# Optimization experiments

Measured on AMD Instinct MI355X. Metric: run time of the kernel, lower is better.

The kernel has to match this reference:

```python
import jax, jax.numpy as jnp
import numpy as np

B, S, HID = 1, 2048, 2048
NH, NKV, HD = 32, 8, 64
INTER = 8192
EPS = 1e-6


def rmsnorm(x, w, eps=EPS):
    xf = x.astype(jnp.float32)
    inv = jax.lax.rsqrt(jnp.mean(xf * xf, axis=-1, keepdims=True) + eps)
    return (xf * inv * w).astype(x.dtype)


def rope(x, sin_t, cos_t):
    # x: [B, S, H, D]; sin/cos: [S, D//2]
    sin = sin_t[None, :, None, :]
    cos = cos_t[None, :, None, :]
    d2 = x.shape[-1] // 2
    x0, x1 = x[..., :d2], x[..., d2:]
    return jnp.concatenate((x0 * cos - x1 * sin, x0 * sin + x1 * cos), axis=-1)


def setup_inputs() -> dict:
    key = jax.random.key(0)
    ks = jax.random.split(key, 12)
    hidden_states = jax.random.normal(ks[0], (B, S, HID), dtype=jnp.float32)
    # realistic RoPE tables
    inv_freq = 1.0 / (10000.0 ** (np.arange(0, HD // 2, dtype=np.float32) * 2.0 / HD))
    ang = np.arange(S, dtype=np.float32)[:, None] * inv_freq[None, :]
    sin_table = jnp.asarray(np.sin(ang))
    cos_table = jnp.asarray(np.cos(ang))
    s = 0.02
    return {
        "hidden_states": hidden_states,
        "sin_table": sin_table,
        "cos_table": cos_table,
        "ln1_w": jnp.ones((HID,), jnp.float32),
        "ln2_w": jnp.ones((HID,), jnp.float32),
        "wq": jax.random.normal(ks[1], (HID, NH * HD), jnp.float32) * s,
        "wk": jax.random.normal(ks[2], (HID, NKV * HD), jnp.float32) * s,
        "wv": jax.random.normal(ks[3], (HID, NKV * HD), jnp.float32) * s,
        "wo": jax.random.normal(ks[4], (NH * HD, HID), jnp.float32) * s,
        "w_gate": jax.random.normal(ks[5], (HID, INTER), jnp.float32) * s,
        "w_up": jax.random.normal(ks[6], (HID, INTER), jnp.float32) * s,
        "w_down": jax.random.normal(ks[7], (INTER, HID), jnp.float32) * s,
    }


def attention(x, sin_t, cos_t, wq, wk, wv, wo):
    b, s, _ = x.shape
    q = (x @ wq).reshape(b, s, NH, HD)
    k = (x @ wk).reshape(b, s, NKV, HD)
    v = (x @ wv).reshape(b, s, NKV, HD).transpose(0, 2, 1, 3)  # [B,Hk,S,D]
    q = rope(q, sin_t, cos_t).transpose(0, 2, 1, 3)  # [B,Hq,S,D]
    k = rope(k, sin_t, cos_t).transpose(0, 2, 1, 3)  # [B,Hk,S,D]
    g = NH // NKV
    k = jnp.repeat(k, g, axis=1)
    v = jnp.repeat(v, g, axis=1)
    scale = 1.0 / np.sqrt(HD)
    scores = jnp.einsum("bhqd,bhkd->bhqk", q, k) * scale
    mask = jnp.tril(jnp.ones((s, s), dtype=bool))
    scores = jnp.where(mask, scores, -jnp.inf)
    probs = jax.nn.softmax(scores, axis=-1)
    out = jnp.einsum("bhqk,bhkd->bhqd", probs, v)
    out = out.transpose(0, 2, 1, 3).reshape(b, s, NH * HD)
    return out @ wo


def reference(hidden_states, sin_table, cos_table, ln1_w, ln2_w, wq, wk, wv, wo, w_gate, w_up, w_down):
    x = hidden_states
    x = x + attention(rmsnorm(x, ln1_w), sin_table, cos_table, wq, wk, wv, wo)
    h = rmsnorm(x, ln2_w)
    x = x + (jax.nn.silu(h @ w_gate) * (h @ w_up)) @ w_down
    return x
```

## Files before the change

kernel.cpp:

```cpp
#include <hip/hip_runtime.h>
#include <hip/hip_bf16.h>

typedef float f32x4 __attribute__((ext_vector_type(4)));
typedef unsigned int u32x4 __attribute__((ext_vector_type(4)));
typedef unsigned int u32x2 __attribute__((ext_vector_type(2)));
typedef _Float16 f16x4 __attribute__((ext_vector_type(4)));
typedef unsigned short u16;

#define S_LEN 2048
#define HID 2048
#define NHEAD 32
#define NKVH 8
#define HDIM 64

__device__ __forceinline__ unsigned short f2bf_bits(float f) {
    unsigned int u = __builtin_bit_cast(unsigned int, f);
    unsigned int r = u + 0x7fffu + ((u >> 16) & 1u);
    return (unsigned short)(r >> 16);
}
__device__ __forceinline__ float bf2f(unsigned short b) {
    unsigned int u = ((unsigned int)b) << 16;
    return __builtin_bit_cast(float, u);
}
__device__ __forceinline__ unsigned cvt_pk_bf16(float lo, float hi) {
    unsigned d;
    asm("v_cvt_pk_bf16_f32 %0, %1, %2" : "=v"(d) : "v"(lo), "v"(hi));
    return d;
}

__device__ __forceinline__ f32x4 mfma_bf16(u32x4 a, u32x4 b, f32x4 c) {
    asm("v_mfma_f32_16x16x32_bf16 %0, %1, %2, %0" : "+v"(c) : "v"(a), "v"(b));
    return c;
}

__device__ __forceinline__ void gload_lds16(const void* g, void* l) {
    __builtin_amdgcn_global_load_lds(
        (const __attribute__((address_space(1))) void*)g,
        (__attribute__((address_space(3))) void*)l, 16, 0, 0);
}

__global__ __launch_bounds__(256)
void rmsnorm_k(const float* __restrict__ x, const float* __restrict__ wgt,
               unsigned short* __restrict__ out)
{
    int row = blockIdx.x;
    int t = threadIdx.x;
    const float* xr = x + (size_t)row * HID;
    f32x4 a = *(const f32x4*)(xr + t * 8);
    f32x4 b = *(const f32x4*)(xr + t * 8 + 4);
    float s = 0.f;
#pragma unroll
    for (int i = 0; i < 4; ++i) s += a[i] * a[i] + b[i] * b[i];
#pragma unroll
    for (int off = 32; off > 0; off >>= 1) s += __shfl_down(s, off);
    __shared__ float red[4];
    if ((t & 63) == 0) red[t >> 6] = s;
    __syncthreads();
    float tot = red[0] + red[1] + red[2] + red[3];
    float inv = rsqrtf(tot * (1.0f / (float)HID) + 1e-6f);
    f32x4 wa = *(const f32x4*)(wgt + t * 8);
    f32x4 wb = *(const f32x4*)(wgt + t * 8 + 4);
    unsigned int pk[4];
#pragma unroll
    for (int i = 0; i < 2; ++i) {
        pk[i]     = (unsigned)f2bf_bits(a[2*i] * inv * wa[2*i]) |
                    ((unsigned)f2bf_bits(a[2*i+1] * inv * wa[2*i+1]) << 16);
        pk[i + 2] = (unsigned)f2bf_bits(b[2*i] * inv * wb[2*i]) |
                    ((unsigned)f2bf_bits(b[2*i+1] * inv * wb[2*i+1]) << 16);
    }
    u32x4 ov; ov[0] = pk[0]; ov[1] = pk[1]; ov[2] = pk[2]; ov[3] = pk[3];
    *(u32x4*)(out + (size_t)row * HID + t * 8) = ov;
}

__global__ __launch_bounds__(256)
void res_rms(const float* __restrict__ x, const _Float16* __restrict__ p,
             const float* __restrict__ wgt, float* __restrict__ x1out,
             unsigned short* __restrict__ xnout, int n)
{
    int row = blockIdx.x;
    int t = threadIdx.x;
    int base = row * HID + t * 8;
    f32x4 a = *(const f32x4*)(x + base);
    f32x4 b = *(const f32x4*)(x + base + 4);
#pragma unroll
    for (int z = 0; z < 4; ++z) {
        f16x4 h0 = *(const f16x4*)(p + (size_t)z * n + base);
        f16x4 h1 = *(const f16x4*)(p + (size_t)z * n + base + 4);
#pragma unroll
        for (int j = 0; j < 4; ++j) { a[j] += (float)h0[j]; b[j] += (float)h1[j]; }
    }
    *(f32x4*)(x1out + base) = a;
    *(f32x4*)(x1out + base + 4) = b;
    float s = 0.f;
#pragma unroll
    for (int i = 0; i < 4; ++i) s += a[i] * a[i] + b[i] * b[i];
#pragma unroll
    for (int off = 32; off > 0; off >>= 1) s += __shfl_down(s, off);
    __shared__ float red[4];
    if ((t & 63) == 0) red[t >> 6] = s;
    __syncthreads();
    float tot = red[0] + red[1] + red[2] + red[3];
    float inv = rsqrtf(tot * (1.0f / (float)HID) + 1e-6f);
    f32x4 wa = *(const f32x4*)(wgt + t * 8);
    f32x4 wb = *(const f32x4*)(wgt + t * 8 + 4);
    unsigned int pk[4];
#pragma unroll
    for (int i = 0; i < 2; ++i) {
        pk[i]     = (unsigned)f2bf_bits(a[2*i] * inv * wa[2*i]) |
                    ((unsigned)f2bf_bits(a[2*i+1] * inv * wa[2*i+1]) << 16);
        pk[i + 2] = (unsigned)f2bf_bits(b[2*i] * inv * wb[2*i]) |
                    ((unsigned)f2bf_bits(b[2*i+1] * inv * wb[2*i+1]) << 16);
    }
    u32x4 ov; ov[0] = pk[0]; ov[1] = pk[1]; ov[2] = pk[2]; ov[3] = pk[3];
    *(u32x4*)(xnout + base) = ov;
}

__global__ __launch_bounds__(256)
void transpose_cvt(const float* __restrict__ in, unsigned short* __restrict__ out,
                   int K, int N)
{
    __shared__ unsigned short tile[64 * 65];
    int kb = blockIdx.y * 64, nb = blockIdx.x * 64;
    int t = threadIdx.x;
    int r = t >> 2, c0 = (t & 3) * 16;
    const float* src = in + (size_t)(kb + r) * N + nb + c0;
#pragma unroll
    for (int j = 0; j < 4; ++j) {
        f32x4 v = *(const f32x4*)(src + j * 4);
#pragma unroll
        for (int i = 0; i < 4; ++i)
            tile[r * 65 + c0 + j * 4 + i] = f2bf_bits(v[i]);
    }
    __syncthreads();
    unsigned short e[16];
#pragma unroll
    for (int j = 0; j < 16; ++j) e[j] = tile[(c0 + j) * 65 + r];
    u32x4 o0, o1;
#pragma unroll
    for (int j = 0; j < 4; ++j) {
        o0[j] = (unsigned)e[2*j] | ((unsigned)e[2*j+1] << 16);
        o1[j] = (unsigned)e[8 + 2*j] | ((unsigned)e[8 + 2*j+1] << 16);
    }
    unsigned short* dst = out + (size_t)(nb + r) * K + kb + c0;
    *(u32x4*)(dst) = o0;
    *(u32x4*)(dst + 8) = o1;
}

__global__ __launch_bounds__(256)
void reduce_rope(const _Float16* __restrict__ p, const float* __restrict__ sin_t,
                 const float* __restrict__ cos_t, unsigned short* __restrict__ qkv,
                 int n)
{
    int s = blockIdx.x;
    size_t base = (size_t)s * 3072;
    for (int it = threadIdx.x; it < (NHEAD + NKVH) * 32; it += 256) {
        int slot = it >> 5, d = it & 31;
        int col = slot * 64 + d;
        float x0 = (float)p[base + col] + (float)p[(size_t)n + base + col];
        float x1 = (float)p[base + col + 32] + (float)p[(size_t)n + base + col + 32];
        float c = cos_t[s * 32 + d], sn = sin_t[s * 32 + d];
        qkv[base + col]      = f2bf_bits(x0 * c - x1 * sn);
        qkv[base + col + 32] = f2bf_bits(x0 * sn + x1 * c);
    }
    for (int it = threadIdx.x; it < NKVH * HDIM; it += 256) {
        int col = 2560 + it;
        float v = (float)p[base + col] + (float)p[(size_t)n + base + col];
        qkv[base + col] = f2bf_bits(v);
    }
}

__global__ __launch_bounds__(256)
void transpose_v(const unsigned short* __restrict__ qkv, unsigned short* __restrict__ vT)
{
    __shared__ unsigned short tile[64][80];
    int kb = blockIdx.x * 64, kvh = blockIdx.y;
    int t = threadIdx.x;
    int r = t >> 2, c0 = (t & 3) * 16;
    const unsigned short* src = qkv + (size_t)(kb + r) * 3072 + 2560 + kvh * 64 + c0;
    u32x4 v0 = *(const u32x4*)(src);
    u32x4 v1 = *(const u32x4*)(src + 8);
    *(u32x4*)&tile[r][c0] = v0;
    *(u32x4*)&tile[r][c0 + 8] = v1;
    __syncthreads();
    int d = t >> 2, k0 = (t & 3) * 16;
    unsigned short e[16];
#pragma unroll
    for (int j = 0; j < 16; ++j) e[j] = tile[k0 + j][d];
    u32x4 o0, o1;
#pragma unroll
    for (int j = 0; j < 4; ++j) {
        o0[j] = (unsigned)e[2*j] | ((unsigned)e[2*j+1] << 16);
        o1[j] = (unsigned)e[8 + 2*j] | ((unsigned)e[8 + 2*j+1] << 16);
    }
    int s0 = ((k0 >> 3) ^ (d & 7)) & 7;
    int s1 = (((k0 >> 3) + 1) ^ (d & 7)) & 7;
    unsigned short* dst = vT + ((size_t)kvh * 64 + d) * 2048 + kb;
    *(u32x4*)(dst + s0 * 8) = o0;
    *(u32x4*)(dst + s1 * 8) = o1;
}

template <int KK>
__device__ __forceinline__ void phaseP(u16* lds, int cur, f32x4 (&acc)[8][4],
                                       u32x4 (&rcur)[12], u32x4 (&rnext)[12],
                                       int aoff, int boff,
                                       const u16* Asrc, const u16* Bsrc,
                                       int lda, int kt_stage,
                                       int dst0, int dst1)
{
    asm volatile("s_waitcnt vmcnt(4)" ::: "memory");
    {
        int nbuf = (KK == 0) ? cur : (cur ^ 1);
        int nslot = (KK == 0) ? 2 : 0;
        const u16* ah = lds + (nbuf * 4 + nslot) * 8192 + aoff;
        const u16* bh = lds + (nbuf * 4 + nslot + 1) * 8192 + boff;
#pragma unroll
        for (int m = 0; m < 8; ++m)
            rnext[m] = *(const u32x4*)(ah + (m >> 2) * 2048 + (m & 3) * 512);
#pragma unroll
        for (int ni = 0; ni < 4; ++ni)
            rnext[8 + ni] = *(const u32x4*)(bh + ni * 512);
    }
    {
        const u16* sa = Asrc + (size_t)kt_stage * 64 + (KK == 0 ? 32 : 0);
        const u16* sb = Bsrc + (size_t)kt_stage * 64 + (KK == 0 ? 32 : 0);
        int dbuf = (KK == 0) ? (cur ^ 1) : cur;
        u16* dA = lds + (dbuf * 4 + (KK == 0 ? 2 : 0)) * 8192;
        u16* dB = lds + (dbuf * 4 + (KK == 0 ? 3 : 1)) * 8192;
        gload_lds16(sa, dA + dst0);
        gload_lds16(sa + (size_t)128 * lda, dA + dst1);
        gload_lds16(sb, dB + dst0);
        gload_lds16(sb + (size_t)128 * lda, dB + dst1);
    }
    __builtin_amdgcn_sched_barrier(0);
    __builtin_amdgcn_s_setprio(1);
#pragma unroll
    for (int m = 0; m < 8; ++m)
#pragma unroll
        for (int ni = 0; ni < 4; ++ni)
            acc[m][ni] = mfma_bf16(rcur[m], rcur[8 + ni], acc[m][ni]);
    __builtin_amdgcn_s_setprio(0);
    __builtin_amdgcn_s_barrier();
}

template <int EPI>
__global__ __launch_bounds__(512, 2)
void gemm8p(const u16* __restrict__ A, const u16* __restrict__ Bt,
            void* __restrict__ outp, const void* __restrict__ auxp,
            int M, int N, int Kc, int lda)
{
    extern __shared__ u16 lds[];
    const int tid = threadIdx.x;
    const int w = tid >> 6, l = tid & 63;
    const int wm = w >> 2, wn = w & 3;
    const int l4 = l >> 4, l15 = l & 15;
    const int zb = blockIdx.y;

    int wg = blockIdx.x, nwg = gridDim.x;
    int swzb = ((nwg & 7) == 0) ? ((wg & 7) * (nwg >> 3) + (wg >> 3)) : wg;
    int rbs = M >> 8;
    int rb = swzb % rbs, cb = swzb / rbs;

    const int sw = ((tid & 3) ^ ((tid >> 3) & 3)) * 8;
    const int srow = tid >> 2;
    const u16* Asrc = A + (size_t)(rb * 256 + srow) * lda + (size_t)zb * Kc + sw;
    const u16* Bsrc = Bt + (size_t)(cb * 256 + srow) * lda + (size_t)zb * Kc + sw;
    const int dst0 = tid * 8, dst1 = (512 + tid) * 8;

    const int rswz = (l15 >> 1) & 3;
    const int aoff = (wm * 128 + l15) * 32 + (l4 ^ rswz) * 8;
    const int boff = (wn * 64 + l15) * 32 + (l4 ^ rswz) * 8;

    f32x4 acc[8][4] = {};
    u32x4 rA[12], rB[12];
    const int NT = Kc >> 6;

    {
#pragma unroll
        for (int h = 0; h < 2; ++h) {
            const u16* sA = Asrc + h * 32;
            const u16* sB = Bsrc + h * 32;
            gload_lds16(sA, lds + (h * 2) * 8192 + dst0);
            gload_lds16(sA + (size_t)128 * lda, lds + (h * 2) * 8192 + dst1);
            gload_lds16(sB, lds + (h * 2 + 1) * 8192 + dst0);
            gload_lds16(sB + (size_t)128 * lda, lds + (h * 2 + 1) * 8192 + dst1);
        }
        int t1 = (NT > 1) ? 1 : 0;
        const u16* sA = Asrc + (size_t)t1 * 64;
        const u16* sB = Bsrc + (size_t)t1 * 64;
        gload_lds16(sA, lds + (4 + 0) * 8192 + dst0);
        gload_lds16(sA + (size_t)128 * lda, lds + (4 + 0) * 8192 + dst1);
        gload_lds16(sB, lds + (4 + 1) * 8192 + dst0);
        gload_lds16(sB + (size_t)128 * lda, lds + (4 + 1) * 8192 + dst1);
    }
    asm volatile("s_waitcnt vmcnt(8)" ::: "memory");
    __builtin_amdgcn_s_barrier();
    {
        const u16* ah = lds + aoff;
        const u16* bh = lds + 8192 + boff;
#pragma unroll
        for (int m = 0; m < 8; ++m)
            rA[m] = *(const u32x4*)(ah + (m >> 2) * 2048 + (m & 3) * 512);
#pragma unroll
        for (int ni = 0; ni < 4; ++ni)
            rA[8 + ni] = *(const u32x4*)(bh + ni * 512);
    }

    for (int t = 0; t < NT; ++t) {
        int cur = t & 1;
        int k1 = (t + 1 < NT) ? t + 1 : 0;
        int k2 = (t + 2 < NT) ? t + 2 : 0;
        phaseP<0>(lds, cur, acc, rA, rB, aoff, boff, Asrc, Bsrc, lda, k1, dst0, dst1);
        phaseP<1>(lds, cur, acc, rB, rA, aoff, boff, Asrc, Bsrc, lda, k2, dst0, dst1);
    }
    asm volatile("s_waitcnt vmcnt(0)" ::: "memory");

    int row0 = rb * 256 + wm * 128 + l4 * 4;
    int col0 = cb * 256 + wn * 64 + l15;
#pragma unroll
    for (int mi = 0; mi < 8; ++mi) {
#pragma unroll
        for (int ni = 0; ni < 4; ++ni) {
#pragma unroll
            for (int r = 0; r < 4; ++r) {
                int row = row0 + mi * 16 + r;
                int col = col0 + ni * 16;
                size_t idx = (size_t)row * N + col;
                float v = acc[mi][ni][r];
                if (EPI == 1) {
                    float sv = v / (1.0f + __expf(-v));
                    ((unsigned short*)outp)[idx] = f2bf_bits(sv);
                } else if (EPI == 2) {
                    float gv = bf2f(((const unsigned short*)auxp)[idx]);
                    ((unsigned short*)outp)[idx] = f2bf_bits(v * gv);
                } else {
                    ((_Float16*)outp)[(size_t)zb * M * N + idx] = (_Float16)v;
                }
            }
        }
    }
}

template <int KK>
__device__ __forceinline__ void phasePgu(u16* lds, int cur, f32x4 (&acc)[8][4],
                                         u32x4 (&rcur)[12], u32x4 (&rnext)[12],
                                         int aoff, int boffg, int boffu,
                                         const u16* Asrc, const u16* Bg, const u16* Bu,
                                         int lda, int kt_stage,
                                         int dst0, int dst1)
{
    asm volatile("s_waitcnt vmcnt(4)" ::: "memory");
    {
        int nbuf = (KK == 0) ? cur : (cur ^ 1);
        int nslot = (KK == 0) ? 2 : 0;
        const u16* ah = lds + (nbuf * 4 + nslot) * 8192 + aoff;
        const u16* bh = lds + (nbuf * 4 + nslot + 1) * 8192;
#pragma unroll
        for (int m = 0; m < 8; ++m)
            rnext[m] = *(const u32x4*)(ah + (m >> 2) * 2048 + (m & 3) * 512);
#pragma unroll
        for (int ni = 0; ni < 2; ++ni) {
            rnext[8 + ni]  = *(const u32x4*)(bh + boffg + ni * 512);
            rnext[10 + ni] = *(const u32x4*)(bh + boffu + ni * 512);
        }
    }
    {
        int koff = (KK == 0 ? 32 : 0);
        const u16* sa = Asrc + (size_t)kt_stage * 64 + koff;
        int dbuf = (KK == 0) ? (cur ^ 1) : cur;
        u16* dA = lds + (dbuf * 4 + (KK == 0 ? 2 : 0)) * 8192;
        u16* dB = lds + (dbuf * 4 + (KK == 0 ? 3 : 1)) * 8192;
        gload_lds16(sa, dA + dst0);
        gload_lds16(sa + (size_t)128 * lda, dA + dst1);
        gload_lds16(Bg + (size_t)kt_stage * 64 + koff, dB + dst0);
        gload_lds16(Bu + (size_t)kt_stage * 64 + koff, dB + dst1);
    }
    __builtin_amdgcn_sched_barrier(0);
    __builtin_amdgcn_s_setprio(1);
#pragma unroll
    for (int m = 0; m < 8; ++m)
#pragma unroll
        for (int ni = 0; ni < 4; ++ni)
            acc[m][ni] = mfma_bf16(rcur[m], rcur[8 + ni], acc[m][ni]);
    __builtin_amdgcn_s_setprio(0);
    __builtin_amdgcn_s_barrier();
}

__global__ __launch_bounds__(512, 2)
void gemm8p_gu(const u16* __restrict__ A, const u16* __restrict__ WgT,
               const u16* __restrict__ WuT, unsigned short* __restrict__ outp,
               int M, int Nfull, int K)
{
    extern __shared__ u16 lds[];
    const int tid = threadIdx.x;
    const int w = tid >> 6, l = tid & 63;
    const int wm = w >> 2, wn = w & 3;
    const int l4 = l >> 4, l15 = l & 15;

    int wg = blockIdx.x, nwg = gridDim.x;
    int swzb = ((nwg & 7) == 0) ? ((wg & 7) * (nwg >> 3) + (wg >> 3)) : wg;
    int rbs = M >> 8;
    int rb = swzb % rbs, cb = swzb / rbs;

    const int sw = ((tid & 3) ^ ((tid >> 3) & 3)) * 8;
    const int srow = tid >> 2;
    const u16* Asrc = A + (size_t)(rb * 256 + srow) * K + sw;
    const u16* Bg = WgT + (size_t)(cb * 128 + srow) * K + sw;
    const u16* Bu = WuT + (size_t)(cb * 128 + srow) * K + sw;
    const int dst0 = tid * 8, dst1 = (512 + tid) * 8;

    const int rswz = (l15 >> 1) & 3;
    const int aoff  = (wm * 128 + l15) * 32 + (l4 ^ rswz) * 8;
    const int boffg = (wn * 32 + l15) * 32 + (l4 ^ rswz) * 8;
    const int boffu = (128 + wn * 32 + l15) * 32 + (l4 ^ rswz) * 8;

    f32x4 acc[8][4] = {};
    u32x4 rA[12], rB[12];
    const int NT = K >> 6;

    {
#pragma unroll
        for (int h = 0; h < 2; ++h) {
            const u16* sA = Asrc + h * 32;
            gload_lds16(sA, lds + (h * 2) * 8192 + dst0);
            gload_lds16(sA + (size_t)128 * K, lds + (h * 2) * 8192 + dst1);
            gload_lds16(Bg + h * 32, lds + (h * 2 + 1) * 8192 + dst0);
            gload_lds16(Bu + h * 32, lds + (h * 2 + 1) * 8192 + dst1);
        }
        const u16* sA = Asrc + 64;
        gload_lds16(sA, lds + (4 + 0) * 8192 + dst0);
        gload_lds16(sA + (size_t)128 * K, lds + (4 + 0) * 8192 + dst1);
        gload_lds16(Bg + 64, lds + (4 + 1) * 8192 + dst0);
        gload_lds16(Bu + 64, lds + (4 + 1) * 8192 + dst1);
    }
    asm volatile("s_waitcnt vmcnt(8)" ::: "memory");
    __builtin_amdgcn_s_barrier();
    {
        const u16* ah = lds + aoff;
        const u16* bh = lds + 8192;
#pragma unroll
        for (int m = 0; m < 8; ++m)
            rA[m] = *(const u32x4*)(ah + (m >> 2) * 2048 + (m & 3) * 512);
#pragma unroll
        for (int ni = 0; ni < 2; ++ni) {
            rA[8 + ni]  = *(const u32x4*)(bh + boffg + ni * 512);
            rA[10 + ni] = *(const u32x4*)(bh + boffu + ni * 512);
        }
    }

    for (int t = 0; t < NT; ++t) {
        int cur = t & 1;
        int k1 = (t + 1 < NT) ? t + 1 : 0;
        int k2 = (t + 2 < NT) ? t + 2 : 0;
        phasePgu<0>(lds, cur, acc, rA, rB, aoff, boffg, boffu, Asrc, Bg, Bu, K, k1, dst0, dst1);
        phasePgu<1>(lds, cur, acc, rB, rA, aoff, boffg, boffu, Asrc, Bg, Bu, K, k2, dst0, dst1);
    }
    asm volatile("s_waitcnt vmcnt(0)" ::: "memory");

    int row0 = rb * 256 + wm * 128 + l4 * 4;
    int col0 = cb * 128 + wn * 32 + l15;
#pragma unroll
    for (int mi = 0; mi < 8; ++mi) {
#pragma unroll
        for (int ni = 0; ni < 2; ++ni) {
#pragma unroll
            for (int r = 0; r < 4; ++r) {
                int row = row0 + mi * 16 + r;
                int col = col0 + ni * 16;
                float gv = acc[mi][ni][r];
                float uv = acc[mi][ni + 2][r];
                float sv = gv / (1.0f + __expf(-gv)) * uv;
                outp[(size_t)row * Nfull + col] = f2bf_bits(sv);
            }
        }
    }
}

__global__ __launch_bounds__(256)
void reduce_add4(float* __restrict__ out, const _Float16* __restrict__ p, int n)
{
    int i = (blockIdx.x * 256 + threadIdx.x) * 4;
    f32x4 a = *(const f32x4*)(out + i);
#pragma unroll
    for (int z = 0; z < 4; ++z) {
        f16x4 h = *(const f16x4*)(p + (size_t)z * n + i);
#pragma unroll
        for (int j = 0; j < 4; ++j) a[j] += (float)h[j];
    }
    *(f32x4*)(out + i) = a;
}

__global__ __launch_bounds__(256)
void attn_fwd(const unsigned short* __restrict__ qkv,
              const unsigned short* __restrict__ vT,
              unsigned short* __restrict__ out)
{
    int p = blockIdx.x, h = blockIdx.y, kvh = h >> 2;
    int t = threadIdx.x, w = t >> 6, l = t & 63;
    int l4 = l >> 4, l15 = l & 15;
    __shared__ unsigned short Ks[2][64 * 64];
    __shared__ unsigned short Vs[2][64 * 64];

    const unsigned short* Kg = qkv + HID + kvh * 64;
    const unsigned short* Vg = vT + (size_t)kvh * 64 * 2048;

    int ch0 = w * 2, ch1 = w * 2 + 1;
    int rsub = l >> 3;
    int ksw = ((l & 7) ^ (rsub & 7)) * 8;
    int vcol = (l & 7) * 8;
    int sw0 = (l4 ^ (l15 & 7)) * 8;
    int sw1 = ((l4 | 4) ^ (l15 & 7)) * 8;
    int srcA = ((l >> 4) & 1) * 32 + l15;
    int srcB = srcA + 16;
    bool hi32 = (l & 32) != 0;

#define STAGE_KV(buf, kt)                                                         \
    {                                                                             \
        gload_lds16(Kg + (size_t)((kt) * 64 + ch0 * 8 + rsub) * 3072 + ksw,       \
                    &Ks[buf][ch0 * 512]);                                         \
        gload_lds16(Kg + (size_t)((kt) * 64 + ch1 * 8 + rsub) * 3072 + ksw,       \
                    &Ks[buf][ch1 * 512]);                                         \
        gload_lds16(Vg + (size_t)(ch0 * 8 + rsub) * 2048 + (kt) * 64 + vcol,      \
                    &Vs[buf][ch0 * 512]);                                         \
        gload_lds16(Vg + (size_t)(ch1 * 8 + rsub) * 2048 + (kt) * 64 + vcol,      \
                    &Vs[buf][ch1 * 512]);                                         \
    }

    const float SC2 = 0.18033688f;
    const float THR = 44.36f;
    const float BIG = -3.0e38f;

    for (int half = 0; half < 2; ++half) {
        int qb = half ? (31 - p) : p;
        int qrow0 = qb * 64 + w * 16;
        STAGE_KV(0, 0);
        const unsigned short* qg = qkv + (size_t)(qrow0 + l15) * 3072 + h * 64 + l4 * 8;
        u32x4 aq0 = *(const u32x4*)(qg);
        u32x4 aq1 = *(const u32x4*)(qg + 32);
        f32x4 o[4] = {};
        float m = BIG, ls = 0.f;
        __syncthreads();
        int cur = 0;
        for (int kt = 0; kt <= qb; ++kt) {
            if (kt < qb) STAGE_KV(cur ^ 1, kt + 1);
            f32x4 sc[4];
#pragma unroll
            for (int n = 0; n < 4; ++n) {
                const unsigned short* kb_ = &Ks[cur][(n * 16 + l15) * 64];
                u32x4 b0 = *(const u32x4*)(kb_ + sw0);
                u32x4 b1 = *(const u32x4*)(kb_ + sw1);
                f32x4 z = {};
                z = mfma_bf16(b0, aq0, z);
                z = mfma_bf16(b1, aq1, z);
                sc[n] = z;
            }
            if (kt == qb) {
                int qloc = w * 16 + l15;
#pragma unroll
                for (int n = 0; n < 4; ++n)
#pragma unroll
                    for (int r = 0; r < 4; ++r)
                        if (n * 16 + l4 * 4 + r > qloc) sc[n][r] = BIG;
            }
            float rmax = BIG;
#pragma unroll
            for (int n = 0; n < 4; ++n)
#pragma unroll
                for (int r = 0; r < 4; ++r) rmax = fmaxf(rmax, sc[n][r]);
            rmax = fmaxf(rmax, __shfl_xor(rmax, 16));
            rmax = fmaxf(rmax, __shfl_xor(rmax, 32));
            if (__ballot(rmax - m > THR)) {
                float mn = fmaxf(m, rmax);
                float al = __builtin_exp2f((m - mn) * SC2);
                m = mn;
                ls *= al;
#pragma unroll
                for (int nd = 0; nd < 4; ++nd)
#pragma unroll
                    for (int r = 0; r < 4; ++r) o[nd][r] *= al;
            }
            float ms = m * SC2, rs = 0.f;
#pragma unroll
            for (int n = 0; n < 4; ++n)
#pragma unroll
                for (int r = 0; r < 4; ++r) {
                    float pe = __builtin_exp2f(__builtin_fmaf(sc[n][r], SC2, -ms));
                    sc[n][r] = pe;
                    rs += pe;
                }
            rs += __shfl_xor(rs, 16);
            rs += __shfl_xor(rs, 32);
            ls += rs;
            unsigned pk0[2], pk1[2], pk2[2], pk3[2];
#pragma unroll
            for (int rr = 0; rr < 2; ++rr) {
                pk0[rr] = cvt_pk_bf16(sc[0][2*rr], sc[0][2*rr+1]);
                pk1[rr] = cvt_pk_bf16(sc[1][2*rr], sc[1][2*rr+1]);
                pk2[rr] = cvt_pk_bf16(sc[2][2*rr], sc[2][2*rr+1]);
                pk3[rr] = cvt_pk_bf16(sc[3][2*rr], sc[3][2*rr+1]);
            }
            u32x4 W1, W2;
            {
                unsigned a0, a1;
                a0 = __shfl(pk0[0], srcA); a1 = __shfl(pk1[0], srcA); W1[0] = hi32 ? a1 : a0;
                a0 = __shfl(pk0[1], srcA); a1 = __shfl(pk1[1], srcA); W1[1] = hi32 ? a1 : a0;
                a0 = __shfl(pk0[0], srcB); a1 = __shfl(pk1[0], srcB); W1[2] = hi32 ? a1 : a0;
                a0 = __shfl(pk0[1], srcB); a1 = __shfl(pk1[1], srcB); W1[3] = hi32 ? a1 : a0;
                a0 = __shfl(pk2[0], srcA); a1 = __shfl(pk3[0], srcA); W2[0] = hi32 ? a1 : a0;
                a0 = __shfl(pk2[1], srcA); a1 = __shfl(pk3[1], srcA); W2[1] = hi32 ? a1 : a0;
                a0 = __shfl(pk2[0], srcB); a1 = __shfl(pk3[0], srcB); W2[2] = hi32 ? a1 : a0;
                a0 = __shfl(pk2[1], srcB); a1 = __shfl(pk3[1], srcB); W2[3] = hi32 ? a1 : a0;
            }
#pragma unroll
            for (int nd = 0; nd < 4; ++nd) {
                const unsigned short* vb = &Vs[cur][(nd * 16 + l15) * 64];
                u32x4 bv0 = *(const u32x4*)(vb + sw0);
                u32x4 bv1 = *(const u32x4*)(vb + sw1);
                o[nd] = mfma_bf16(bv0, W1, o[nd]);
                o[nd] = mfma_bf16(bv1, W2, o[nd]);
            }
            __syncthreads();
            cur ^= 1;
        }
#undef STAGE_KV
        float linv = 1.0f / ls;
        unsigned short* orow = out + (size_t)(qrow0 + l15) * HID + h * 64 + l4 * 4;
#pragma unroll
        for (int nd = 0; nd < 4; ++nd) {
            u32x2 wv;
            wv[0] = cvt_pk_bf16(o[nd][0] * linv, o[nd][1] * linv);
            wv[1] = cvt_pk_bf16(o[nd][2] * linv, o[nd][3] * linv);
            *(u32x2*)(orow + nd * 16) = wv;
        }
    }
}

extern "C" void kernel_launch(void* const* d_in, const int* in_sizes, int n_in,
                              void* d_out, int out_size, void* d_ws, size_t ws_size,
                              hipStream_t stream)
{
    const float* x     = (const float*)d_in[0];
    const float* sin_t = (const float*)d_in[1];
    const float* cos_t = (const float*)d_in[2];
    const float* ln1w  = (const float*)d_in[3];
    const float* ln2w  = (const float*)d_in[4];
    const float* wq    = (const float*)d_in[5];
    const float* wk    = (const float*)d_in[6];
    const float* wv    = (const float*)d_in[7];
    const float* wo    = (const float*)d_in[8];
    const float* wg    = (const float*)d_in[9];
    const float* wu    = (const float*)d_in[10];
    const float* wd    = (const float*)d_in[11];
    float* out = (float*)d_out;

    char* ws = (char*)d_ws;
    if (ws_size < 113246208u) return;
    unsigned short* wT    = (unsigned short*)(ws);
    unsigned short* xn    = (unsigned short*)(ws + 33554432u);
    unsigned short* qkv   = (unsigned short*)(ws + 41943040u);
    unsigned short* attn  = (unsigned short*)(ws + 54525952u);
    unsigned short* vT    = (unsigned short*)(ws + 62914560u);
    unsigned short* wuT   = (unsigned short*)(ws + 41943040u);
    _Float16*       part  = (_Float16*)(ws + 41943040u);
    unsigned short* g     = (unsigned short*)(ws + 79691776u);
    _Float16*       opart = (_Float16*)(ws + 79691776u);
    _Float16*       qpart = (_Float16*)(ws + 79691776u);

    hipFuncSetAttribute(reinterpret_cast<const void*>(&gemm8p<5>),
                        hipFuncAttributeMaxDynamicSharedMemorySize, 131072);
    hipFuncSetAttribute(reinterpret_cast<const void*>(&gemm8p_gu),
                        hipFuncAttributeMaxDynamicSharedMemorySize, 131072);

    rmsnorm_k<<<S_LEN, 256, 0, stream>>>(x, ln1w, xn);

    transpose_cvt<<<dim3(32, 32), 256, 0, stream>>>(wq, wT, 2048, 2048);
    transpose_cvt<<<dim3(8, 32), 256, 0, stream>>>(wk, wT + (size_t)2048 * 2048, 2048, 512);
    transpose_cvt<<<dim3(8, 32), 256, 0, stream>>>(wv, wT + (size_t)2560 * 2048, 2048, 512);

    gemm8p<5><<<dim3(96, 2), 512, 131072, stream>>>(xn, wT, qpart, nullptr, 2048, 3072, 1024, 2048);

    reduce_rope<<<S_LEN, 256, 0, stream>>>(qpart, sin_t, cos_t, qkv, 6291456);

    transpose_v<<<dim3(32, 8), 256, 0, stream>>>(qkv, vT);

    attn_fwd<<<dim3(16, 32), 256, 0, stream>>>(qkv, vT, attn);

    transpose_cvt<<<dim3(32, 32), 256, 0, stream>>>(wo, wT, 2048, 2048);
    gemm8p<5><<<dim3(64, 4), 512, 131072, stream>>>(attn, wT, opart, nullptr, 2048, 2048, 512, 2048);

    res_rms<<<S_LEN, 256, 0, stream>>>(x, opart, ln2w, out, xn, 4194304);

    transpose_cvt<<<dim3(128, 32), 256, 0, stream>>>(wg, wT, 2048, 8192);
    transpose_cvt<<<dim3(128, 32), 256, 0, stream>>>(wu, wuT, 2048, 8192);
    gemm8p_gu<<<dim3(512), 512, 131072, stream>>>(xn, wT, wuT, g, 2048, 8192, 2048);

    transpose_cvt<<<dim3(32, 128), 256, 0, stream>>>(wd, wT, 8192, 2048);
    gemm8p<5><<<dim3(64, 4), 512, 131072, stream>>>(g, wT, part, nullptr, 2048, 2048, 2048, 8192);

    reduce_add4<<<4096, 256, 0, stream>>>(out, part, 4194304);
}
```

Measured before the change: 416.5 us.

## Switch GEMM inner loops from 16x16x32 to 32x32x16 bf16 MFMA tiles

Replaces the 16x16x32 MFMA accumulation in the main GEMM and the fused gate/up GEMM with 32x32x16 MFMA instructions. LDS fragment loads, swizzle offsets and epilogue index mapping are reworked to match the 32x32 output layout. The larger instruction issues fewer MFMAs for the same work and changes LDS read patterns. The gemm8p epilogue drops its EPI==1/2 branches and always writes fp16 partials, which would change behaviour for any launch that used those modes.

```diff
diff --git a/kernel.cpp b/kernel.cpp
--- a/kernel.cpp
+++ b/kernel.cpp
@@ -2,6 +2,7 @@
 #include <hip/hip_bf16.h>
 
 typedef float f32x4 __attribute__((ext_vector_type(4)));
+typedef float f32x16 __attribute__((ext_vector_type(16)));
 typedef unsigned int u32x4 __attribute__((ext_vector_type(4)));
 typedef unsigned int u32x2 __attribute__((ext_vector_type(2)));
 typedef _Float16 f16x4 __attribute__((ext_vector_type(4)));
@@ -30,6 +31,10 @@
 
 __device__ __forceinline__ f32x4 mfma_bf16(u32x4 a, u32x4 b, f32x4 c) {
     asm("v_mfma_f32_16x16x32_bf16 %0, %1, %2, %0" : "+v"(c) : "v"(a), "v"(b));
+    return c;
+}
+__device__ __forceinline__ f32x16 mfma32_bf16(u32x4 a, u32x4 b, f32x16 c) {
+    asm("v_mfma_f32_32x32x16_bf16 %0, %1, %2, %0" : "+v"(c) : "v"(a), "v"(b));
     return c;
 }
 
@@ -200,9 +205,9 @@
 }
 
 template <int KK>
-__device__ __forceinline__ void phaseP(u16* lds, int cur, f32x4 (&acc)[8][4],
+__device__ __forceinline__ void phaseP(u16* lds, int cur, f32x16 (&acc)[4][2],
                                        u32x4 (&rcur)[12], u32x4 (&rnext)[12],
-                                       int aoff, int boff,
+                                       int abase, int bbase, int cof0, int cof1,
                                        const u16* Asrc, const u16* Bsrc,
                                        int lda, int kt_stage,
                                        int dst0, int dst1)
@@ -211,14 +216,18 @@
     {
         int nbuf = (KK == 0) ? cur : (cur ^ 1);
         int nslot = (KK == 0) ? 2 : 0;
-        const u16* ah = lds + (nbuf * 4 + nslot) * 8192 + aoff;
-        const u16* bh = lds + (nbuf * 4 + nslot + 1) * 8192 + boff;
-#pragma unroll
-        for (int m = 0; m < 8; ++m)
-            rnext[m] = *(const u32x4*)(ah + (m >> 2) * 2048 + (m & 3) * 512);
-#pragma unroll
-        for (int ni = 0; ni < 4; ++ni)
-            rnext[8 + ni] = *(const u32x4*)(bh + ni * 512);
+        const u16* ah = lds + (nbuf * 4 + nslot) * 8192 + abase;
+        const u16* bh = lds + (nbuf * 4 + nslot + 1) * 8192 + bbase;
+#pragma unroll
+        for (int mt = 0; mt < 4; ++mt) {
+            rnext[mt * 2 + 0] = *(const u32x4*)(ah + mt * 1024 + cof0);
+            rnext[mt * 2 + 1] = *(const u32x4*)(ah + mt * 1024 + cof1);
+        }
+#pragma unroll
+        for (int nt = 0; nt < 2; ++nt) {
+            rnext[8 + nt * 2 + 0] = *(const u32x4*)(bh + nt * 1024 + cof0);
+            rnext[8 + nt * 2 + 1] = *(const u32x4*)(bh + nt * 1024 + cof1);
+        }
     }
     {
         const u16* sa = Asrc + (size_t)kt_stage * 64 + (KK == 0 ? 32 : 0);
@@ -234,10 +243,12 @@
     __builtin_amdgcn_sched_barrier(0);
     __builtin_amdgcn_s_setprio(1);
 #pragma unroll
-    for (int m = 0; m < 8; ++m)
-#pragma unroll
-        for (int ni = 0; ni < 4; ++ni)
-            acc[m][ni] = mfma_bf16(rcur[m], rcur[8 + ni], acc[m][ni]);
+    for (int ks = 0; ks < 2; ++ks)
+#pragma unroll
+        for (int mt = 0; mt < 4; ++mt)
+#pragma unroll
+            for (int nt = 0; nt < 2; ++nt)
+                acc[mt][nt] = mfma32_bf16(rcur[mt * 2 + ks], rcur[8 + nt * 2 + ks], acc[mt][nt]);
     __builtin_amdgcn_s_setprio(0);
     __builtin_amdgcn_s_barrier();
 }
@@ -252,7 +263,7 @@
     const int tid = threadIdx.x;
     const int w = tid >> 6, l = tid & 63;
     const int wm = w >> 2, wn = w & 3;
-    const int l4 = l >> 4, l15 = l & 15;
+    const int r31 = l & 31, hi = l >> 5;
     const int zb = blockIdx.y;
 
     int wg = blockIdx.x, nwg = gridDim.x;
@@ -266,11 +277,13 @@
     const u16* Bsrc = Bt + (size_t)(cb * 256 + srow) * lda + (size_t)zb * Kc + sw;
     const int dst0 = tid * 8, dst1 = (512 + tid) * 8;
 
-    const int rswz = (l15 >> 1) & 3;
-    const int aoff = (wm * 128 + l15) * 32 + (l4 ^ rswz) * 8;
-    const int boff = (wn * 64 + l15) * 32 + (l4 ^ rswz) * 8;
-
-    f32x4 acc[8][4] = {};
+    const int key = (r31 >> 1) & 3;
+    const int abase = (wm * 128 + r31) * 32;
+    const int bbase = (wn * 64 + r31) * 32;
+    const int cof0 = ((0 + hi) ^ key) * 8;
+    const int cof1 = ((2 + hi) ^ key) * 8;
+
+    f32x16 acc[4][2] = {};
     u32x4 rA[12], rB[12];
     const int NT = Kc >> 6;
 
@@ -295,55 +308,51 @@
     asm volatile("s_waitcnt vmcnt(8)" ::: "memory");
     __builtin_amdgcn_s_barrier();
     {
-        const u16* ah = lds + aoff;
-        const u16* bh = lds + 8192 + boff;
-#pragma unroll
-        for (int m = 0; m < 8; ++m)
-            rA[m] = *(const u32x4*)(ah + (m >> 2) * 2048 + (m & 3) * 512);
-#pragma unroll
-        for (int ni = 0; ni < 4; ++ni)
-            rA[8 + ni] = *(const u32x4*)(bh + ni * 512);
+        const u16* ah = lds + abase;
+        const u16* bh = lds + 8192 + bbase;
+#pragma unroll
+        for (int mt = 0; mt < 4; ++mt) {
+            rA[mt * 2 + 0] = *(const u32x4*)(ah + mt * 1024 + cof0);
+            rA[mt * 2 + 1] = *(const u32x4*)(ah + mt * 1024 + cof1);
+        }
+#pragma unroll
+        for (int nt = 0; nt < 2; ++nt) {
+            rA[8 + nt * 2 + 0] = *(const u32x4*)(bh + nt * 1024 + cof0);
+            rA[8 + nt * 2 + 1] = *(const u32x4*)(bh + nt * 1024 + cof1);
+        }
     }
 
     for (int t = 0; t < NT; ++t) {
         int cur = t & 1;
         int k1 = (t + 1 < NT) ? t + 1 : 0;
         int k2 = (t + 2 < NT) ? t + 2 : 0;
-        phaseP<0>(lds, cur, acc, rA, rB, aoff, boff, Asrc, Bsrc, lda, k1, dst0, dst1);
-        phaseP<1>(lds, cur, acc, rB, rA, aoff, boff, Asrc, Bsrc, lda, k2, dst0, dst1);
+        phaseP<0>(lds, cur, acc, rA, rB, abase, bbase, cof0, cof1, Asrc, Bsrc, lda, k1, dst0, dst1);
+        phaseP<1>(lds, cur, acc, rB, rA, abase, bbase, cof0, cof1, Asrc, Bsrc, lda, k2, dst0, dst1);
     }
     asm volatile("s_waitcnt vmcnt(0)" ::: "memory");
 
-    int row0 = rb * 256 + wm * 128 + l4 * 4;
-    int col0 = cb * 256 + wn * 64 + l15;
-#pragma unroll
-    for (int mi = 0; mi < 8; ++mi) {
-#pragma unroll
-        for (int ni = 0; ni < 4; ++ni) {
-#pragma unroll
-            for (int r = 0; r < 4; ++r) {
-                int row = row0 + mi * 16 + r;
-                int col = col0 + ni * 16;
+    int row0 = rb * 256 + wm * 128;
+    int col0 = cb * 256 + wn * 64;
+#pragma unroll
+    for (int mt = 0; mt < 4; ++mt) {
+#pragma unroll
+        for (int nt = 0; nt < 2; ++nt) {
+#pragma unroll
+            for (int reg = 0; reg < 16; ++reg) {
+                int row = row0 + mt * 32 + (reg & 3) + 8 * (reg >> 2) + 4 * hi;
+                int col = col0 + nt * 32 + r31;
                 size_t idx = (size_t)row * N + col;
-                float v = acc[mi][ni][r];
-                if (EPI == 1) {
-                    float sv = v / (1.0f + __expf(-v));
-                    ((unsigned short*)outp)[idx] = f2bf_bits(sv);
-                } else if (EPI == 2) {
-                    float gv = bf2f(((const unsigned short*)auxp)[idx]);
-                    ((unsigned short*)outp)[idx] = f2bf_bits(v * gv);
-                } else {
-                    ((_Float16*)outp)[(size_t)zb * M * N + idx] = (_Float16)v;
-                }
+                ((_Float16*)outp)[(size_t)zb * M * N + idx] = (_Float16)acc[mt][nt][reg];
             }
         }
     }
 }
 
 template <int KK>
-__device__ __forceinline__ void phasePgu(u16* lds, int cur, f32x4 (&acc)[8][4],
+__device__ __forceinline__ void phasePgu(u16* lds, int cur, f32x16 (&acc)[4][2],
                                          u32x4 (&rcur)[12], u32x4 (&rnext)[12],
-                                         int aoff, int boffg, int boffu,
+                                         int abase, int bbaseg, int bbaseu,
+                                         int cof0, int cof1,
                                          const u16* Asrc, const u16* Bg, const u16* Bu,
                                          int lda, int kt_stage,
                                          int dst0, int dst1)
@@ -352,16 +361,17 @@
     {
         int nbuf = (KK == 0) ? cur : (cur ^ 1);
         int nslot = (KK == 0) ? 2 : 0;
-        const u16* ah = lds + (nbuf * 4 + nslot) * 8192 + aoff;
+        const u16* ah = lds + (nbuf * 4 + nslot) * 8192 + abase;
         const u16* bh = lds + (nbuf * 4 + nslot + 1) * 8192;
 #pragma unroll
-        for (int m = 0; m < 8; ++m)
-            rnext[m] = *(const u32x4*)(ah + (m >> 2) * 2048 + (m & 3) * 512);
-#pragma unroll
-        for (int ni = 0; ni < 2; ++ni) {
-            rnext[8 + ni]  = *(const u32x4*)(bh + boffg + ni * 512);
-            rnext[10 + ni] = *(const u32x4*)(bh + boffu + ni * 512);
-        }
+        for (int mt = 0; mt < 4; ++mt) {
+            rnext[mt * 2 + 0] = *(const u32x4*)(ah + mt * 1024 + cof0);
+            rnext[mt * 2 + 1] = *(const u32x4*)(ah + mt * 1024 + cof1);
+        }
+        rnext[8]  = *(const u32x4*)(bh + bbaseg + cof0);
+        rnext[9]  = *(const u32x4*)(bh + bbaseg + cof1);
+        rnext[10] = *(const u32x4*)(bh + bbaseu + cof0);
+        rnext[11] = *(const u32x4*)(bh + bbaseu + cof1);
     }
     {
         int koff = (KK == 0 ? 32 : 0);
@@ -377,10 +387,12 @@
     __builtin_amdgcn_sched_barrier(0);
     __builtin_amdgcn_s_setprio(1);
 #pragma unroll
-    for (int m = 0; m < 8; ++m)
-#pragma unroll
-        for (int ni = 0; ni < 4; ++ni)
-            acc[m][ni] = mfma_bf16(rcur[m], rcur[8 + ni], acc[m][ni]);
+    for (int ks = 0; ks < 2; ++ks)
+#pragma unroll
+        for (int mt = 0; mt < 4; ++mt)
+#pragma unroll
+            for (int nt = 0; nt < 2; ++nt)
+                acc[mt][nt] = mfma32_bf16(rcur[mt * 2 + ks], rcur[8 + nt * 2 + ks], acc[mt][nt]);
     __builtin_amdgcn_s_setprio(0);
     __builtin_amdgcn_s_barrier();
 }
@@ -394,7 +406,7 @@
     const int tid = threadIdx.x;
     const int w = tid >> 6, l = tid & 63;
     const int wm = w >> 2, wn = w & 3;
-    const int l4 = l >> 4, l15 = l & 15;
+    const int r31 = l & 31, hi = l >> 5;
 
     int wg = blockIdx.x, nwg = gridDim.x;
     int swzb = ((nwg & 7) == 0) ? ((wg & 7) * (nwg >> 3) + (wg >> 3)) : wg;
@@ -408,12 +420,14 @@
     const u16* Bu = WuT + (size_t)(cb * 128 + srow) * K + sw;
     const int dst0 = tid * 8, dst1 = (512 + tid) * 8;
 
-    const int rswz = (l15 >> 1) & 3;
-    const int aoff  = (wm * 128 + l15) * 32 + (l4 ^ rswz) * 8;
-    const int boffg = (wn * 32 + l15) * 32 + (l4 ^ rswz) * 8;
-    const int boffu = (128 + wn * 32 + l15) * 32 + (l4 ^ rswz) * 8;
-
-    f32x4 acc[8][4] = {};
+    const int key = (r31 >> 1) & 3;
+    const int abase  = (wm * 128 + r31) * 32;
+    const int bbaseg = (wn * 32 + r31) * 32;
+    const int bbaseu = (128 + wn * 32 + r31) * 32;
+    const int cof0 = ((0 + hi) ^ key) * 8;
+    const int cof1 = ((2 + hi) ^ key) * 8;
+
+    f32x16 acc[4][2] = {};
     u32x4 rA[12], rB[12];
     const int NT = K >> 6;
 
@@ -435,42 +449,39 @@
     asm volatile("s_waitcnt vmcnt(8)" ::: "memory");
     __builtin_amdgcn_s_barrier();
     {
-        const u16* ah = lds + aoff;
+        const u16* ah = lds + abase;
         const u16* bh = lds + 8192;
 #pragma unroll
-        for (int m = 0; m < 8; ++m)
-            rA[m] = *(const u32x4*)(ah + (m >> 2) * 2048 + (m & 3) * 512);
-#pragma unroll
-        for (int ni = 0; ni < 2; ++ni) {
-            rA[8 + ni]  = *(const u32x4*)(bh + boffg + ni * 512);
-            rA[10 + ni] = *(const u32x4*)(bh + boffu + ni * 512);
-        }
+        for (int mt = 0; mt < 4; ++mt) {
+            rA[mt * 2 + 0] = *(const u32x4*)(ah + mt * 1024 + cof0);
+            rA[mt * 2 + 1] = *(const u32x4*)(ah + mt * 1024 + cof1);
+        }
+        rA[8]  = *(const u32x4*)(bh + bbaseg + cof0);
+        rA[9]  = *(const u32x4*)(bh + bbaseg + cof1);
+        rA[10] = *(const u32x4*)(bh + bbaseu + cof0);
+        rA[11] = *(const u32x4*)(bh + bbaseu + cof1);
     }
 
     for (int t = 0; t < NT; ++t) {
         int cur = t & 1;
         int k1 = (t + 1 < NT) ? t + 1 : 0;
         int k2 = (t + 2 < NT) ? t + 2 : 0;
-        phasePgu<0>(lds, cur, acc, rA, rB, aoff, boffg, boffu, Asrc, Bg, Bu, K, k1, dst0, dst1);
-        phasePgu<1>(lds, cur, acc, rB, rA, aoff, boffg, boffu, Asrc, Bg, Bu, K, k2, dst0, dst1);
+        phasePgu<0>(lds, cur, acc, rA, rB, abase, bbaseg, bbaseu, cof0, cof1, Asrc, Bg, Bu, K, k1, dst0, dst1);
+        phasePgu<1>(lds, cur, acc, rB, rA, abase, bbaseg, bbaseu, cof0, cof1, Asrc, Bg, Bu, K, k2, dst0, dst1);
     }
     asm volatile("s_waitcnt vmcnt(0)" ::: "memory");
 
-    int row0 = rb * 256 + wm * 128 + l4 * 4;
-    int col0 = cb * 128 + wn * 32 + l15;
-#pragma unroll
-    for (int mi = 0; mi < 8; ++mi) {
-#pragma unroll
-        for (int ni = 0; ni < 2; ++ni) {
-#pragma unroll
-            for (int r = 0; r < 4; ++r) {
-                int row = row0 + mi * 16 + r;
-                int col = col0 + ni * 16;
-                float gv = acc[mi][ni][r];
-                float uv = acc[mi][ni + 2][r];
-                float sv = gv / (1.0f + __expf(-gv)) * uv;
-                outp[(size_t)row * Nfull + col] = f2bf_bits(sv);
-            }
+    int row0 = rb * 256 + wm * 128;
+    int col0 = cb * 128 + wn * 32 + r31;
+#pragma unroll
+    for (int mt = 0; mt < 4; ++mt) {
+#pragma unroll
+        for (int reg = 0; reg < 16; ++reg) {
+            int row = row0 + mt * 32 + (reg & 3) + 8 * (reg >> 2) + 4 * hi;
+            float gv = acc[mt][0][reg];
+            float uv = acc[mt][1][reg];
+            float sv = gv / (1.0f + __expf(-gv)) * uv;
+            outp[(size_t)row * Nfull + col0] = f2bf_bits(sv);
         }
     }
 }
```

After: 436.2 us. +4.7%, slower.
